# Kernel tuning notes

Hardware: AMD Instinct MI355X
Metric: run time of the kernel (lower is better)

The kernel has to match this reference:

```python
import jax, jax.numpy as jnp
import numpy as np
import math

B, S, D = 2, 2048, 1024
N_HEAD = 16
EPS = 1e-6

def setup_inputs() -> dict:
    key = jax.random.key(0)
    ks = jax.random.split(key, 12)
    def lin(k):
        kw, kb = jax.random.split(k)
        scale = 1.0 / math.sqrt(D)
        W = jax.random.uniform(kw, (D, D), jnp.float32, -scale, scale)
        b = jax.random.uniform(kb, (D,), jnp.float32, -scale, scale)
        return W, b
    Wq, bq = lin(ks[0]); Wk, bk = lin(ks[1]); Wv, bv = lin(ks[2]); Wo, bo = lin(ks[3])
    return {
        'query': jax.random.normal(ks[4], (B, S, D), jnp.float32),
        'key':   jax.random.normal(ks[5], (B, S, D), jnp.float32),
        'value': jax.random.normal(ks[6], (B, S, D), jnp.float32),
        'mask':  jnp.ones((B, S, S), jnp.int32),
        'Wq': Wq, 'bq': bq, 'Wk': Wk, 'bk': bk, 'Wv': Wv, 'bv': bv,
        'Wo': Wo, 'bo': bo,
        'gamma': jnp.ones((D,), jnp.float32),
        'beta':  jnp.zeros((D,), jnp.float32),
    }

def reference(query, key, value, mask, Wq, bq, Wk, bk, Wv, bv, Wo, bo, gamma, beta):
    b, s, dm = query.shape
    h = N_HEAD
    d = dm // h
    residual = query
    # projections (torch Linear: x @ W.T + b) -> [b, h, s, d]
    def proj(x, W, bias):
        return (x @ W.T + bias).reshape(b, -1, h, d).transpose(0, 2, 1, 3)
    q = proj(query, Wq, bq)
    k = proj(key, Wk, bk)
    v = proj(value, Wv, bv)
    scores = jnp.einsum('bhqd,bhkd->bhqk', q, k) / jnp.sqrt(jnp.float32(d))
    scores = jnp.where(mask[:, None, :, :] == 0, jnp.float32(-1e9), scores)
    p_attn = jax.nn.softmax(scores, axis=-1)  # dropout is identity in eval/reference
    x = jnp.einsum('bhqk,bhkd->bhqd', p_attn, v)
    x = x.transpose(0, 2, 1, 3).reshape(b, -1, h * d)
    x = x @ Wo.T + bo
    x = x + residual
    # LayerNorm with unbiased std and (std + eps) denominator, as in source
    mean = jnp.mean(x, axis=-1, keepdims=True)
    std = jnp.std(x, axis=-1, keepdims=True, ddof=1)
    return gamma * (x - mean) / (std + EPS) + beta
```

## Files before the change

kernel.cpp:

```cpp
#include <hip/hip_runtime.h>
#include <hip/hip_bf16.h>
#include <math.h>
#include <stdint.h>

#define BATCH 2
#define SEQ   2048
#define DMODEL 1024
#define NHEAD 16
#define HDIM  64
#define NROWS (BATCH*SEQ)
#define EPS   1e-6f
#define QSCALE 0.1803368801111204f

typedef float f32x4 __attribute__((ext_vector_type(4)));
typedef short s16x8 __attribute__((ext_vector_type(8)));
typedef unsigned int u32x4 __attribute__((ext_vector_type(4)));

#define OFF_XQ 0
#define OFF_XK 4194304
#define OFF_XV 8388608
#define OFF_WQ 12582912
#define OFF_WK 13631488
#define OFF_WV 14680064
#define OFF_WO 15728640
#define OFF_QB 16777216
#define OFF_KB 20971520
#define OFF_VT 25165824
#define OFF_CM 29360128
#define OFF_MS 29884416

__device__ __forceinline__ unsigned short f2bf(float x) {
    unsigned int u = __builtin_bit_cast(unsigned int, x);
    u += 0x7fff + ((u >> 16) & 1);
    return (unsigned short)(u >> 16);
}

__device__ __forceinline__ void gl_lds16(const void* g, void* l) {
    __builtin_amdgcn_global_load_lds(
        (const __attribute__((address_space(1))) unsigned int*)g,
        (__attribute__((address_space(3))) unsigned int*)(unsigned int)(unsigned long long)l,
        16, 0, 0);
}

__global__ __launch_bounds__(256) void conv_all_kernel(
    const float* __restrict__ q, const float* __restrict__ k, const float* __restrict__ v,
    const float* __restrict__ wq, const float* __restrict__ wk, const float* __restrict__ wv,
    const float* __restrict__ wo, unsigned short* __restrict__ ws)
{
    if (blockIdx.x == 0 && threadIdx.x < 32)
        ((unsigned int*)(ws + OFF_MS))[threadIdx.x] = 0;
    size_t t = ((size_t)blockIdx.x * 256 + threadIdx.x) * 4;
    const float* src; unsigned short* dst; size_t off;
    if (t < 4194304)       { src = q;  dst = ws + OFF_XQ; off = t; }
    else if (t < 8388608)  { src = k;  dst = ws + OFF_XK; off = t - 4194304; }
    else if (t < 12582912) { src = v;  dst = ws + OFF_XV; off = t - 8388608; }
    else if (t < 13631488) { src = wq; dst = ws + OFF_WQ; off = t - 12582912; }
    else if (t < 14680064) { src = wk; dst = ws + OFF_WK; off = t - 13631488; }
    else if (t < 15728640) { src = wv; dst = ws + OFF_WV; off = t - 14680064; }
    else                   { src = wo; dst = ws + OFF_WO; off = t - 15728640; }
    float4 x = *(const float4*)&src[off];
    ushort4 o;
    o.x = f2bf(x.x); o.y = f2bf(x.y); o.z = f2bf(x.z); o.w = f2bf(x.w);
    *(ushort4*)&dst[off] = o;
}

__global__ __launch_bounds__(256) void mask_compress_kernel(
    const int* __restrict__ mask, unsigned long long* __restrict__ cm,
    unsigned int* __restrict__ msum)
{
    int t = blockIdx.x * 256 + threadIdx.x;
    int lane = t & 63;
    int w = t >> 6;
    int s  = w & 2047;
    int kb = (w >> 11) & 31;
    int b  = w >> 16;
    int m = mask[((size_t)b * SEQ + s) * SEQ + kb * 64 + lane];
    unsigned long long bits = __ballot(m != 0);
    if (lane == 0) {
        cm[((size_t)b * 32 + kb) * SEQ + s] = bits;
        if (bits != ~0ull)
            atomicOr(&msum[(b << 4) | (s >> 7)], 1u << kb);
    }
}

__device__ __forceinline__ void gemm_body(
    const unsigned short* A, const unsigned short* W, int r0, int c0,
    unsigned short* As, unsigned short* Bs, f32x4 acc[4][4])
{
    const int tid  = threadIdx.x;
    const int wave = tid >> 6, lane = tid & 63;
    const int quad = lane >> 4, l15 = lane & 15;
    const int wr = wave >> 1, wc = wave & 1;
    for (int k0 = 0; k0 < DMODEL; k0 += 64) {
        __syncthreads();
        #pragma unroll
        for (int r = 0; r < 4; r++) {
            int f   = r * 4096 + tid * 16;
            int row = f >> 7;
            int g   = (((f >> 4) & 7) - row) & 7;
            gl_lds16((const char*)A + (size_t)(r0 + row) * 2048 + k0 * 2 + g * 16,
                     (char*)As + r * 4096 + wave * 1024);
            gl_lds16((const char*)W + (size_t)(c0 + row) * 2048 + k0 * 2 + g * 16,
                     (char*)Bs + r * 4096 + wave * 1024);
        }
        __syncthreads();
        #pragma unroll
        for (int ks = 0; ks < 2; ks++) {
            s16x8 a[4], b[4];
            #pragma unroll
            for (int mt = 0; mt < 4; mt++) {
                int row = wr*64 + mt*16 + l15;
                a[mt] = *(const s16x8*)((const char*)As + row * 128 + ((ks*4 + quad + row) & 7) * 16);
            }
            #pragma unroll
            for (int nt = 0; nt < 4; nt++) {
                int row = wc*64 + nt*16 + l15;
                b[nt] = *(const s16x8*)((const char*)Bs + row * 128 + ((ks*4 + quad + row) & 7) * 16);
            }
            #pragma unroll
            for (int mt = 0; mt < 4; mt++)
                #pragma unroll
                for (int nt = 0; nt < 4; nt++)
                    acc[mt][nt] = __builtin_amdgcn_mfma_f32_16x16x32_bf16(a[mt], b[nt], acc[mt][nt], 0, 0, 0);
        }
    }
}

__global__ __launch_bounds__(256) void qkv_gemm_kernel(
    unsigned short* __restrict__ ws,
    const float* __restrict__ bq, const float* __restrict__ bk, const float* __restrict__ bv)
{
    __shared__ __align__(16) unsigned short As[8192];
    __shared__ __align__(16) unsigned short Bs[8192];
    const int z = blockIdx.z;
    const unsigned short *A, *W;
    int r0, c0;
    if (z != 2) {
        A = ws + (size_t)z * 4194304;
        W = ws + OFF_WQ + (size_t)z * 1048576;
        r0 = blockIdx.x * 128; c0 = blockIdx.y * 128;
    } else {
        A = ws + OFF_WV;
        W = ws + OFF_XV;
        r0 = blockIdx.y * 128; c0 = blockIdx.x * 128;
    }
    const float* bias = (z == 0) ? bq : (z == 1 ? bk : bv);
    unsigned short* outp = ws + OFF_QB + (size_t)z * 4194304;
    const float scale = (z == 0) ? QSCALE : 1.0f;

    f32x4 acc[4][4] = {};
    gemm_body(A, W, r0, c0, As, Bs, acc);

    const int lane = threadIdx.x & 63, wave = threadIdx.x >> 6;
    const int quad = lane >> 4, l15 = lane & 15;
    const int wr = wave >> 1, wc = wave & 1;
    if (z != 2) {
        float bias_v[4];
        #pragma unroll
        for (int nt = 0; nt < 4; nt++) bias_v[nt] = bias[c0 + wc*64 + nt*16 + l15];
        #pragma unroll
        for (int mt = 0; mt < 4; mt++) {
            #pragma unroll
            for (int nt = 0; nt < 4; nt++) {
                int c = c0 + wc*64 + nt*16 + l15;
                int hh = c >> 6, dd = c & 63;
                #pragma unroll
                for (int reg = 0; reg < 4; reg++) {
                    int r = r0 + wr*64 + mt*16 + quad*4 + reg;
                    int bb = r >> 11, ss = r & (SEQ - 1);
                    float val = (acc[mt][nt][reg] + bias_v[nt]) * scale;
                    outp[(((size_t)(bb*NHEAD + hh)) * SEQ + ss) * HDIM + dd] = f2bf(val);
                }
            }
        }
    } else {
        #pragma unroll
        for (int mt = 0; mt < 4; mt++) {
            #pragma unroll
            for (int reg = 0; reg < 4; reg++) {
                int f = r0 + wr*64 + mt*16 + quad*4 + reg;
                int hh = f >> 6, dd = f & 63;
                float bfv = bias[f];
                #pragma unroll
                for (int nt = 0; nt < 4; nt++) {
                    int r = c0 + wc*64 + nt*16 + l15;
                    int bb = r >> 11, ss = r & (SEQ - 1);
                    outp[(((size_t)(bb*NHEAD + hh)) * HDIM + dd) * SEQ + ss] =
                        f2bf(acc[mt][nt][reg] + bfv);
                }
            }
        }
    }
}

__global__ __launch_bounds__(256) void oproj_gemm_kernel(
    const unsigned short* __restrict__ ws, const float* __restrict__ bo,
    const float* __restrict__ resid, float* __restrict__ outf)
{
    __shared__ __align__(16) unsigned short As[8192];
    __shared__ __align__(16) unsigned short Bs[8192];
    const unsigned short* A = ws + OFF_XQ;
    const unsigned short* W = ws + OFF_WO;
    const int r0 = blockIdx.x * 128, c0 = blockIdx.y * 128;

    f32x4 acc[4][4] = {};
    gemm_body(A, W, r0, c0, (unsigned short*)As, (unsigned short*)Bs, acc);

    const int lane = threadIdx.x & 63, wave = threadIdx.x >> 6;
    const int quad = lane >> 4, l15 = lane & 15;
    const int wr = wave >> 1, wc = wave & 1;
    #pragma unroll
    for (int mt = 0; mt < 4; mt++) {
        #pragma unroll
        for (int nt = 0; nt < 4; nt++) {
            int c = c0 + wc*64 + nt*16 + l15;
            float bv = bo[c];
            #pragma unroll
            for (int reg = 0; reg < 4; reg++) {
                int r = r0 + wr*64 + mt*16 + quad*4 + reg;
                size_t idx = (size_t)r * DMODEL + c;
                outf[idx] = acc[mt][nt][reg] + bv + resid[idx];
            }
        }
    }
}

__global__ __launch_bounds__(512) void attn_mfma_kernel(
    const unsigned short* __restrict__ ws,
    const unsigned long long* __restrict__ cmask,
    const unsigned int* __restrict__ msum,
    unsigned short* __restrict__ ab)
{
    const int tid  = threadIdx.x;
    const int wave = tid >> 6, lane = tid & 63;
    const int quad = lane >> 4, l15 = lane & 15;
    const int h = blockIdx.y, b = blockIdx.z;
    const int qw = blockIdx.x * 128 + wave * 16;

    const char* qh = (const char*)(ws + OFF_QB + ((size_t)(b*NHEAD + h)) * SEQ * HDIM);
    const char* kh = (const char*)(ws + OFF_KB + ((size_t)(b*NHEAD + h)) * SEQ * HDIM);
    const char* vh = (const char*)(ws + OFF_VT + ((size_t)(b*NHEAD + h)) * SEQ * HDIM);

    __shared__ __align__(16) char Ks[2][2][8192];
    __shared__ __align__(16) char Vs[2][2][8192];

    const unsigned int chunkflags = msum[(b << 4) | blockIdx.x];

    const int srow = tid >> 3;
    const int sgrp = ((tid & 7) - srow) & 7;
    const int arow = (srow & 0x23) | ((srow & 0x0C) << 1) | ((srow & 0x10) >> 2);

    #define STAGE(bfi, k0)                                                           \
        do {                                                                         \
            gl_lds16(kh + (size_t)((k0) + arow) * 128 + sgrp * 16,                   \
                     Ks[bfi][0] + wave * 1024);                                      \
            gl_lds16(kh + (size_t)((k0) + 64 + arow) * 128 + sgrp * 16,              \
                     Ks[bfi][1] + wave * 1024);                                      \
            gl_lds16(vh + (size_t)srow * 4096 + (size_t)(k0) * 2 + sgrp * 16,        \
                     Vs[bfi][0] + wave * 1024);                                      \
            gl_lds16(vh + (size_t)srow * 4096 + (size_t)((k0) + 64) * 2 + sgrp * 16, \
                     Vs[bfi][1] + wave * 1024);                                      \
        } while (0)

    s16x8 qa[2];
    #pragma unroll
    for (int ks = 0; ks < 2; ks++)
        qa[ks] = *(const s16x8*)(qh + (size_t)(qw + l15) * 128 + ks*64 + quad*16);

    int koff[4][2], voff[4][2];
    #pragma unroll
    for (int kt = 0; kt < 4; kt++) {
        int prow = kt*16 + l15;
        koff[kt][0] = prow*128 + ((quad     + prow) & 7) * 16;
        koff[kt][1] = prow*128 + ((4 + quad + prow) & 7) * 16;
    }
    #pragma unroll
    for (int nt = 0; nt < 4; nt++) {
        int d = nt*16 + l15;
        voff[nt][0] = d*128 + ((quad     + d) & 7) * 16;
        voff[nt][1] = d*128 + ((4 + quad + d) & 7) * 16;
    }

    s16x8 onesf;
    {
        short so = (short)0x3F80;
        if (l15 == 0) onesf = (s16x8){so, so, so, so, so, so, so, so};
        else          onesf = (s16x8){0, 0, 0, 0, 0, 0, 0, 0};
    }

    f32x4 o[4], lsum = {0.f, 0.f, 0.f, 0.f};
    #pragma unroll
    for (int nt = 0; nt < 4; nt++) o[nt] = (f32x4){0.f, 0.f, 0.f, 0.f};

    STAGE(0, 0);
    int bf = 0;
    for (int k0 = 0; k0 < SEQ; k0 += 128) {
        __syncthreads();
        if (k0 + 128 < SEQ) STAGE(bf ^ 1, k0 + 128);

        #pragma unroll
        for (int half = 0; half < 2; half++) {
            const char* Kb = Ks[bf][half];
            const char* Vb = Vs[bf][half];
            const int kc = (k0 >> 6) + half;
            f32x4 st[4];
            #pragma unroll
            for (int kt = 0; kt < 4; kt++) {
                s16x8 kf0 = *(const s16x8*)(Kb + koff[kt][0]);
                s16x8 kf1 = *(const s16x8*)(Kb + koff[kt][1]);
                f32x4 z = {0.f, 0.f, 0.f, 0.f};
                st[kt] = __builtin_amdgcn_mfma_f32_16x16x32_bf16(kf0, qa[0], z, 0, 0, 0);
                st[kt] = __builtin_amdgcn_mfma_f32_16x16x32_bf16(kf1, qa[1], st[kt], 0, 0, 0);
            }
            if (chunkflags & (1u << kc)) {
                unsigned long long cm =
                    cmask[((size_t)b*32 + kc) * SEQ + qw + l15];
                if (cm != ~0ull) {
                    #pragma unroll
                    for (int kt = 0; kt < 4; kt++)
                        #pragma unroll
                        for (int reg = 0; reg < 4; reg++) {
                            int key = (kt >> 1)*32 + quad*8 + (kt & 1)*4 + reg;
                            if (!((cm >> key) & 1)) st[kt][reg] = -1e9f;
                        }
                }
            }
            #pragma unroll
            for (int ks = 0; ks < 2; ks++) {
                unsigned int pb[8];
                #pragma unroll
                for (int j = 0; j < 8; j++) {
                    int kt = 2*ks + (j >> 2), r = j & 3;
                    pb[j] = __builtin_bit_cast(unsigned int, exp2f(st[kt][r]));
                }
                u32x4 pw;
                pw[0] = __builtin_amdgcn_perm(pb[1], pb[0], 0x07060302u);
                pw[1] = __builtin_amdgcn_perm(pb[3], pb[2], 0x07060302u);
                pw[2] = __builtin_amdgcn_perm(pb[5], pb[4], 0x07060302u);
                pw[3] = __builtin_amdgcn_perm(pb[7], pb[6], 0x07060302u);
                s16x8 pa = __builtin_bit_cast(s16x8, pw);
                lsum = __builtin_amdgcn_mfma_f32_16x16x32_bf16(pa, onesf, lsum, 0, 0, 0);
                #pragma unroll
                for (int nt = 0; nt < 4; nt++) {
                    s16x8 vf = *(const s16x8*)(Vb + voff[nt][ks]);
                    o[nt] = __builtin_amdgcn_mfma_f32_16x16x32_bf16(pa, vf, o[nt], 0, 0, 0);
                }
            }
        }
        bf ^= 1;
    }
    #undef STAGE
    #pragma unroll
    for (int reg = 0; reg < 4; reg++) {
        float lv = __shfl(lsum[reg], lane & 48);
        float inv = 1.f / lv;
        int sg = qw + quad*4 + reg;
        #pragma unroll
        for (int nt = 0; nt < 4; nt++) {
            size_t idx = ((size_t)b * SEQ + sg) * DMODEL + h*HDIM + nt*16 + l15;
            ab[idx] = f2bf(o[nt][reg] * inv);
        }
    }
}

__global__ __launch_bounds__(256) void ln_kernel(
    float* __restrict__ x, const float* __restrict__ gamma,
    const float* __restrict__ beta)
{
    const int row = blockIdx.x;
    const int tid = threadIdx.x;
    float4 vals = *(const float4*)&x[(size_t)row * DMODEL + tid * 4];
    float s  = vals.x + vals.y + vals.z + vals.w;
    float ss = vals.x*vals.x + vals.y*vals.y + vals.z*vals.z + vals.w*vals.w;
    #pragma unroll
    for (int off = 32; off > 0; off >>= 1) {
        s  += __shfl_down(s, off);
        ss += __shfl_down(ss, off);
    }
    __shared__ float sbuf[4], ssbuf[4];
    __shared__ float mean_s, inv_s;
    if ((tid & 63) == 0) { sbuf[tid >> 6] = s; ssbuf[tid >> 6] = ss; }
    __syncthreads();
    if (tid == 0) {
        float S1 = 0.f, S2 = 0.f;
        #pragma unroll
        for (int i = 0; i < 4; i++) { S1 += sbuf[i]; S2 += ssbuf[i]; }
        float mean = S1 * (1.0f / DMODEL);
        float var  = (S2 - (float)DMODEL * mean * mean) * (1.0f / (DMODEL - 1));
        float sd   = sqrtf(fmaxf(var, 0.f));
        mean_s = mean;
        inv_s  = 1.f / (sd + EPS);
    }
    __syncthreads();
    float4 g  = *(const float4*)&gamma[tid * 4];
    float4 bt = *(const float4*)&beta[tid * 4];
    float4 o;
    o.x = g.x * (vals.x - mean_s) * inv_s + bt.x;
    o.y = g.y * (vals.y - mean_s) * inv_s + bt.y;
    o.z = g.z * (vals.z - mean_s) * inv_s + bt.z;
    o.w = g.w * (vals.w - mean_s) * inv_s + bt.w;
    *(float4*)&x[(size_t)row * DMODEL + tid * 4] = o;
}

extern "C" void kernel_launch(void* const* d_in, const int* in_sizes, int n_in,
                              void* d_out, int out_size, void* d_ws, size_t ws_size,
                              hipStream_t stream) {
    const float* query = (const float*)d_in[0];
    const float* key   = (const float*)d_in[1];
    const float* value = (const float*)d_in[2];
    const int*   mask  = (const int*)d_in[3];
    const float* Wq = (const float*)d_in[4];  const float* bq = (const float*)d_in[5];
    const float* Wk = (const float*)d_in[6];  const float* bk = (const float*)d_in[7];
    const float* Wv = (const float*)d_in[8];  const float* bv = (const float*)d_in[9];
    const float* Wo = (const float*)d_in[10]; const float* bo = (const float*)d_in[11];
    const float* gamma = (const float*)d_in[12];
    const float* beta  = (const float*)d_in[13];
    float* out = (float*)d_out;

    unsigned short* ws = (unsigned short*)d_ws;
    unsigned long long* cmask = (unsigned long long*)(ws + OFF_CM);
    unsigned int* msum = (unsigned int*)(ws + OFF_MS);

    conv_all_kernel<<<16384, 256, 0, stream>>>(query, key, value, Wq, Wk, Wv, Wo, ws);
    mask_compress_kernel<<<32768, 256, 0, stream>>>(mask, cmask, msum);
    qkv_gemm_kernel<<<dim3(32, 8, 3), 256, 0, stream>>>(ws, bq, bk, bv);
    attn_mfma_kernel<<<dim3(SEQ/128, NHEAD, BATCH), 512, 0, stream>>>(ws, cmask, msum, ws + OFF_XQ);
    oproj_gemm_kernel<<<dim3(32, 8), 256, 0, stream>>>(ws, bo, query, out);
    ln_kernel<<<NROWS, 256, 0, stream>>>(out, gamma, beta);
}
```

Before: 283.2 us.

## Split attention key range across two wave groups with LDS merge

Grows the attention block to 1024 threads. Each group of 8 waves processes half of the key sequence for the same 128 queries, so there are twice as many waves in flight to hide latency. The partial outputs and row sums of the second half are combined through shared memory before normalisation. In exchange it uses 64KB of LDS per block, adds an extra merge step with two barriers, and its occupancy hint (1024, 8) may push register limits.

```diff
diff --git a/kernel.cpp b/kernel.cpp
--- a/kernel.cpp
+++ b/kernel.cpp
@@ -225,7 +225,7 @@
     }
 }
 
-__global__ __launch_bounds__(512) void attn_mfma_kernel(
+__global__ __launch_bounds__(1024, 8) void attn_mfma_kernel(
     const unsigned short* __restrict__ ws,
     const unsigned long long* __restrict__ cmask,
     const unsigned int* __restrict__ msum,
@@ -234,32 +234,33 @@
     const int tid  = threadIdx.x;
     const int wave = tid >> 6, lane = tid & 63;
     const int quad = lane >> 4, l15 = lane & 15;
+    const int w8   = wave & 7;
+    const int half = wave >> 3;
     const int h = blockIdx.y, b = blockIdx.z;
-    const int qw = blockIdx.x * 128 + wave * 16;
+    const int qw = blockIdx.x * 128 + w8 * 16;
 
     const char* qh = (const char*)(ws + OFF_QB + ((size_t)(b*NHEAD + h)) * SEQ * HDIM);
     const char* kh = (const char*)(ws + OFF_KB + ((size_t)(b*NHEAD + h)) * SEQ * HDIM);
     const char* vh = (const char*)(ws + OFF_VT + ((size_t)(b*NHEAD + h)) * SEQ * HDIM);
 
-    __shared__ __align__(16) char Ks[2][2][8192];
-    __shared__ __align__(16) char Vs[2][2][8192];
+    __shared__ __align__(16) char smem[65536];
+    char* Kbase = smem + half * 32768;
+    char* Vbase = smem + half * 32768 + 16384;
 
     const unsigned int chunkflags = msum[(b << 4) | blockIdx.x];
 
-    const int srow = tid >> 3;
-    const int sgrp = ((tid & 7) - srow) & 7;
+    const int t512 = tid & 511;
+    const int srow = t512 >> 3;
+    const int sgrp = ((t512 & 7) - srow) & 7;
     const int arow = (srow & 0x23) | ((srow & 0x0C) << 1) | ((srow & 0x10) >> 2);
-
-    #define STAGE(bfi, k0)                                                           \
-        do {                                                                         \
-            gl_lds16(kh + (size_t)((k0) + arow) * 128 + sgrp * 16,                   \
-                     Ks[bfi][0] + wave * 1024);                                      \
-            gl_lds16(kh + (size_t)((k0) + 64 + arow) * 128 + sgrp * 16,              \
-                     Ks[bfi][1] + wave * 1024);                                      \
-            gl_lds16(vh + (size_t)srow * 4096 + (size_t)(k0) * 2 + sgrp * 16,        \
-                     Vs[bfi][0] + wave * 1024);                                      \
-            gl_lds16(vh + (size_t)srow * 4096 + (size_t)((k0) + 64) * 2 + sgrp * 16, \
-                     Vs[bfi][1] + wave * 1024);                                      \
+    const int kb0  = half * 1024;
+
+    #define STAGE(bfi, k0)                                                      \
+        do {                                                                    \
+            gl_lds16(kh + (size_t)((k0) + arow) * 128 + sgrp * 16,              \
+                     Kbase + (bfi) * 8192 + w8 * 1024);                         \
+            gl_lds16(vh + (size_t)srow * 4096 + (size_t)(k0) * 2 + sgrp * 16,   \
+                     Vbase + (bfi) * 8192 + w8 * 1024);                         \
         } while (0)
 
     s16x8 qa[2];
@@ -292,73 +293,95 @@
     #pragma unroll
     for (int nt = 0; nt < 4; nt++) o[nt] = (f32x4){0.f, 0.f, 0.f, 0.f};
 
-    STAGE(0, 0);
+    STAGE(0, kb0);
     int bf = 0;
-    for (int k0 = 0; k0 < SEQ; k0 += 128) {
+    for (int kc = 0; kc < 16; kc++) {
         __syncthreads();
-        if (k0 + 128 < SEQ) STAGE(bf ^ 1, k0 + 128);
-
-        #pragma unroll
-        for (int half = 0; half < 2; half++) {
-            const char* Kb = Ks[bf][half];
-            const char* Vb = Vs[bf][half];
-            const int kc = (k0 >> 6) + half;
-            f32x4 st[4];
-            #pragma unroll
-            for (int kt = 0; kt < 4; kt++) {
-                s16x8 kf0 = *(const s16x8*)(Kb + koff[kt][0]);
-                s16x8 kf1 = *(const s16x8*)(Kb + koff[kt][1]);
-                f32x4 z = {0.f, 0.f, 0.f, 0.f};
-                st[kt] = __builtin_amdgcn_mfma_f32_16x16x32_bf16(kf0, qa[0], z, 0, 0, 0);
-                st[kt] = __builtin_amdgcn_mfma_f32_16x16x32_bf16(kf1, qa[1], st[kt], 0, 0, 0);
-            }
-            if (chunkflags & (1u << kc)) {
-                unsigned long long cm =
-                    cmask[((size_t)b*32 + kc) * SEQ + qw + l15];
-                if (cm != ~0ull) {
+        if (kc + 1 < 16) STAGE(bf ^ 1, kb0 + (kc + 1) * 64);
+
+        const char* Kb = Kbase + bf * 8192;
+        const char* Vb = Vbase + bf * 8192;
+        const int kcg = (half << 4) + kc;
+        f32x4 st[4];
+        #pragma unroll
+        for (int kt = 0; kt < 4; kt++) {
+            s16x8 kf0 = *(const s16x8*)(Kb + koff[kt][0]);
+            s16x8 kf1 = *(const s16x8*)(Kb + koff[kt][1]);
+            f32x4 z = {0.f, 0.f, 0.f, 0.f};
+            st[kt] = __builtin_amdgcn_mfma_f32_16x16x32_bf16(kf0, qa[0], z, 0, 0, 0);
+            st[kt] = __builtin_amdgcn_mfma_f32_16x16x32_bf16(kf1, qa[1], st[kt], 0, 0, 0);
+        }
+        if (chunkflags & (1u << kcg)) {
+            unsigned long long cm =
+                cmask[((size_t)b*32 + kcg) * SEQ + qw + l15];
+            if (cm != ~0ull) {
+                #pragma unroll
+                for (int kt = 0; kt < 4; kt++)
                     #pragma unroll
-                    for (int kt = 0; kt < 4; kt++)
-                        #pragma unroll
-                        for (int reg = 0; reg < 4; reg++) {
-                            int key = (kt >> 1)*32 + quad*8 + (kt & 1)*4 + reg;
-                            if (!((cm >> key) & 1)) st[kt][reg] = -1e9f;
-                        }
-                }
-            }
-            #pragma unroll
-            for (int ks = 0; ks < 2; ks++) {
-                unsigned int pb[8];
-                #pragma unroll
-                for (int j = 0; j < 8; j++) {
-                    int kt = 2*ks + (j >> 2), r = j & 3;
-                    pb[j] = __builtin_bit_cast(unsigned int, exp2f(st[kt][r]));
-                }
-                u32x4 pw;
-                pw[0] = __builtin_amdgcn_perm(pb[1], pb[0], 0x07060302u);
-                pw[1] = __builtin_amdgcn_perm(pb[3], pb[2], 0x07060302u);
-                pw[2] = __builtin_amdgcn_perm(pb[5], pb[4], 0x07060302u);
-                pw[3] = __builtin_amdgcn_perm(pb[7], pb[6], 0x07060302u);
-                s16x8 pa = __builtin_bit_cast(s16x8, pw);
-                lsum = __builtin_amdgcn_mfma_f32_16x16x32_bf16(pa, onesf, lsum, 0, 0, 0);
-                #pragma unroll
-                for (int nt = 0; nt < 4; nt++) {
-                    s16x8 vf = *(const s16x8*)(Vb + voff[nt][ks]);
-                    o[nt] = __builtin_amdgcn_mfma_f32_16x16x32_bf16(pa, vf, o[nt], 0, 0, 0);
-                }
+                    for (int reg = 0; reg < 4; reg++) {
+                        int key = (kt >> 1)*32 + quad*8 + (kt & 1)*4 + reg;
+                        if (!((cm >> key) & 1)) st[kt][reg] = -1e9f;
+                    }
+            }
+        }
+        #pragma unroll
+        for (int ks = 0; ks < 2; ks++) {
+            unsigned int pb[8];
+            #pragma unroll
+            for (int j = 0; j < 8; j++) {
+                int kt = 2*ks + (j >> 2), r = j & 3;
+                pb[j] = __builtin_bit_cast(unsigned int, exp2f(st[kt][r]));
+            }
+            u32x4 pw;
+            pw[0] = __builtin_amdgcn_perm(pb[1], pb[0], 0x07060302u);
+            pw[1] = __builtin_amdgcn_perm(pb[3], pb[2], 0x07060302u);
+            pw[2] = __builtin_amdgcn_perm(pb[5], pb[4], 0x07060302u);
+            pw[3] = __builtin_amdgcn_perm(pb[7], pb[6], 0x07060302u);
+            s16x8 pa = __builtin_bit_cast(s16x8, pw);
+            lsum = __builtin_amdgcn_mfma_f32_16x16x32_bf16(pa, onesf, lsum, 0, 0, 0);
+            #pragma unroll
+            for (int nt = 0; nt < 4; nt++) {
+                s16x8 vf = *(const s16x8*)(Vb + voff[nt][ks]);
+                o[nt] = __builtin_amdgcn_mfma_f32_16x16x32_bf16(pa, vf, o[nt], 0, 0, 0);
             }
         }
         bf ^= 1;
     }
     #undef STAGE
-    #pragma unroll
-    for (int reg = 0; reg < 4; reg++) {
-        float lv = __shfl(lsum[reg], lane & 48);
-        float inv = 1.f / lv;
-        int sg = qw + quad*4 + reg;
-        #pragma unroll
-        for (int nt = 0; nt < 4; nt++) {
-            size_t idx = ((size_t)b * SEQ + sg) * DMODEL + h*HDIM + nt*16 + l15;
-            ab[idx] = f2bf(o[nt][reg] * inv);
+
+    __syncthreads();
+    float* mbuf = (float*)smem;
+    const int mslot = (w8 * 64 + lane) * 21;
+    if (half == 1) {
+        #pragma unroll
+        for (int nt = 0; nt < 4; nt++)
+            #pragma unroll
+            for (int reg = 0; reg < 4; reg++)
+                mbuf[mslot + nt*4 + reg] = o[nt][reg];
+        #pragma unroll
+        for (int reg = 0; reg < 4; reg++)
+            mbuf[mslot + 16 + reg] = lsum[reg];
+    }
+    __syncthreads();
+    if (half == 0) {
+        #pragma unroll
+        for (int nt = 0; nt < 4; nt++)
+            #pragma unroll
+            for (int reg = 0; reg < 4; reg++)
+                o[nt][reg] += mbuf[mslot + nt*4 + reg];
+        #pragma unroll
+        for (int reg = 0; reg < 4; reg++)
+            lsum[reg] += mbuf[mslot + 16 + reg];
+        #pragma unroll
+        for (int reg = 0; reg < 4; reg++) {
+            float lv = __shfl(lsum[reg], lane & 48);
+            float inv = 1.f / lv;
+            int sg = qw + quad*4 + reg;
+            #pragma unroll
+            for (int nt = 0; nt < 4; nt++) {
+                size_t idx = ((size_t)b * SEQ + sg) * DMODEL + h*HDIM + nt*16 + l15;
+                ab[idx] = f2bf(o[nt][reg] * inv);
+            }
         }
     }
 }
@@ -424,7 +447,7 @@
     conv_all_kernel<<<16384, 256, 0, stream>>>(query, key, value, Wq, Wk, Wv, Wo, ws);
     mask_compress_kernel<<<32768, 256, 0, stream>>>(mask, cmask, msum);
     qkv_gemm_kernel<<<dim3(32, 8, 3), 256, 0, stream>>>(ws, bq, bk, bv);
-    attn_mfma_kernel<<<dim3(SEQ/128, NHEAD, BATCH), 512, 0, stream>>>(ws, cmask, msum, ws + OFF_XQ);
+    attn_mfma_kernel<<<dim3(SEQ/128, NHEAD, BATCH), 1024, 0, stream>>>(ws, cmask, msum, ws + OFF_XQ);
     oproj_gemm_kernel<<<dim3(32, 8), 256, 0, stream>>>(ws, bo, query, out);
     ln_kernel<<<NROWS, 256, 0, stream>>>(out, gamma, beta);
 }
```

New measurement: 311.2 us. 9.9% more time.

## Fold mask compression into QKV GEMM launch and simplify LDS fragment addressing

Applied to the files above, without the earlier changes.

The separate mask_compress kernel is removed. Its work now runs in an extra z-slice (z==3) of the QKV GEMM grid, where 256 blocks each scan 512 mask rows with a per-wave loop, overlapping the mask read with the GEMM blocks and saving one launch. Swizzled LDS offsets in the GEMM and attention kernels are also rewritten as base offset plus constant stride, which relies on the row-based swizzle term being invariant across 16-row tiles. This cuts address arithmetic and registers. The risk is that the 64 MB mask read now competes with the GEMM for bandwidth, and the fewer mask blocks may have less parallelism.

```diff
diff --git a/kernel.cpp b/kernel.cpp
--- a/kernel.cpp
+++ b/kernel.cpp
@@ -64,25 +64,6 @@
     *(ushort4*)&dst[off] = o;
 }
 
-__global__ __launch_bounds__(256) void mask_compress_kernel(
-    const int* __restrict__ mask, unsigned long long* __restrict__ cm,
-    unsigned int* __restrict__ msum)
-{
-    int t = blockIdx.x * 256 + threadIdx.x;
-    int lane = t & 63;
-    int w = t >> 6;
-    int s  = w & 2047;
-    int kb = (w >> 11) & 31;
-    int b  = w >> 16;
-    int m = mask[((size_t)b * SEQ + s) * SEQ + kb * 64 + lane];
-    unsigned long long bits = __ballot(m != 0);
-    if (lane == 0) {
-        cm[((size_t)b * 32 + kb) * SEQ + s] = bits;
-        if (bits != ~0ull)
-            atomicOr(&msum[(b << 4) | (s >> 7)], 1u << kb);
-    }
-}
-
 __device__ __forceinline__ void gemm_body(
     const unsigned short* A, const unsigned short* W, int r0, int c0,
     unsigned short* As, unsigned short* Bs, f32x4 acc[4][4])
@@ -91,6 +72,10 @@
     const int wave = tid >> 6, lane = tid & 63;
     const int quad = lane >> 4, l15 = lane & 15;
     const int wr = wave >> 1, wc = wave & 1;
+    const int aBase0 = (wr*64 + l15)*128 + ((    quad + l15) & 7)*16;
+    const int aBase1 = (wr*64 + l15)*128 + ((4 + quad + l15) & 7)*16;
+    const int bBase0 = (wc*64 + l15)*128 + ((    quad + l15) & 7)*16;
+    const int bBase1 = (wc*64 + l15)*128 + ((4 + quad + l15) & 7)*16;
     for (int k0 = 0; k0 < DMODEL; k0 += 64) {
         __syncthreads();
         #pragma unroll
@@ -106,17 +91,15 @@
         __syncthreads();
         #pragma unroll
         for (int ks = 0; ks < 2; ks++) {
+            const int aB = ks ? aBase1 : aBase0;
+            const int bB = ks ? bBase1 : bBase0;
             s16x8 a[4], b[4];
             #pragma unroll
-            for (int mt = 0; mt < 4; mt++) {
-                int row = wr*64 + mt*16 + l15;
-                a[mt] = *(const s16x8*)((const char*)As + row * 128 + ((ks*4 + quad + row) & 7) * 16);
-            }
-            #pragma unroll
-            for (int nt = 0; nt < 4; nt++) {
-                int row = wc*64 + nt*16 + l15;
-                b[nt] = *(const s16x8*)((const char*)Bs + row * 128 + ((ks*4 + quad + row) & 7) * 16);
-            }
+            for (int mt = 0; mt < 4; mt++)
+                a[mt] = *(const s16x8*)((const char*)As + aB + mt*2048);
+            #pragma unroll
+            for (int nt = 0; nt < 4; nt++)
+                b[nt] = *(const s16x8*)((const char*)Bs + bB + nt*2048);
             #pragma unroll
             for (int mt = 0; mt < 4; mt++)
                 #pragma unroll
@@ -128,11 +111,35 @@
 
 __global__ __launch_bounds__(256) void qkv_gemm_kernel(
     unsigned short* __restrict__ ws,
-    const float* __restrict__ bq, const float* __restrict__ bk, const float* __restrict__ bv)
-{
+    const float* __restrict__ bq, const float* __restrict__ bk, const float* __restrict__ bv,
+    const int* __restrict__ mask)
+{
+    const int z = blockIdx.z;
+    if (z == 3) {
+        unsigned long long* cm = (unsigned long long*)(ws + OFF_CM);
+        unsigned int* msum = (unsigned int*)(ws + OFF_MS);
+        const int lane = threadIdx.x & 63;
+        const int wv = threadIdx.x >> 6;
+        const int bid = blockIdx.y * 32 + blockIdx.x;
+        const int wbase = (bid * 4 + wv) * 128;
+        for (int i = 0; i < 128; i++) {
+            int w = wbase + i;
+            int s  = w & 2047;
+            int kb = (w >> 11) & 31;
+            int b  = w >> 16;
+            int m = mask[((size_t)b * SEQ + s) * SEQ + kb * 64 + lane];
+            unsigned long long bits = __ballot(m != 0);
+            if (lane == 0) {
+                cm[((size_t)b * 32 + kb) * SEQ + s] = bits;
+                if (bits != ~0ull)
+                    atomicOr(&msum[(b << 4) | (s >> 7)], 1u << kb);
+            }
+        }
+        return;
+    }
+
     __shared__ __align__(16) unsigned short As[8192];
     __shared__ __align__(16) unsigned short Bs[8192];
-    const int z = blockIdx.z;
     const unsigned short *A, *W;
     int r0, c0;
     if (z != 2) {
@@ -267,19 +274,8 @@
     for (int ks = 0; ks < 2; ks++)
         qa[ks] = *(const s16x8*)(qh + (size_t)(qw + l15) * 128 + ks*64 + quad*16);
 
-    int koff[4][2], voff[4][2];
-    #pragma unroll
-    for (int kt = 0; kt < 4; kt++) {
-        int prow = kt*16 + l15;
-        koff[kt][0] = prow*128 + ((quad     + prow) & 7) * 16;
-        koff[kt][1] = prow*128 + ((4 + quad + prow) & 7) * 16;
-    }
-    #pragma unroll
-    for (int nt = 0; nt < 4; nt++) {
-        int d = nt*16 + l15;
-        voff[nt][0] = d*128 + ((quad     + d) & 7) * 16;
-        voff[nt][1] = d*128 + ((4 + quad + d) & 7) * 16;
-    }
+    const int fbaseA = l15*128 + ((    quad + l15) & 7) * 16;
+    const int fbaseB = l15*128 + ((4 + quad + l15) & 7) * 16;
 
     s16x8 onesf;
     {
@@ -306,8 +302,8 @@
             f32x4 st[4];
             #pragma unroll
             for (int kt = 0; kt < 4; kt++) {
-                s16x8 kf0 = *(const s16x8*)(Kb + koff[kt][0]);
-                s16x8 kf1 = *(const s16x8*)(Kb + koff[kt][1]);
+                s16x8 kf0 = *(const s16x8*)(Kb + fbaseA + kt*2048);
+                s16x8 kf1 = *(const s16x8*)(Kb + fbaseB + kt*2048);
                 f32x4 z = {0.f, 0.f, 0.f, 0.f};
                 st[kt] = __builtin_amdgcn_mfma_f32_16x16x32_bf16(kf0, qa[0], z, 0, 0, 0);
                 st[kt] = __builtin_amdgcn_mfma_f32_16x16x32_bf16(kf1, qa[1], st[kt], 0, 0, 0);
@@ -340,9 +336,10 @@
                 pw[3] = __builtin_amdgcn_perm(pb[7], pb[6], 0x07060302u);
                 s16x8 pa = __builtin_bit_cast(s16x8, pw);
                 lsum = __builtin_amdgcn_mfma_f32_16x16x32_bf16(pa, onesf, lsum, 0, 0, 0);
+                const int fb = (ks == 0) ? fbaseA : fbaseB;
                 #pragma unroll
                 for (int nt = 0; nt < 4; nt++) {
-                    s16x8 vf = *(const s16x8*)(Vb + voff[nt][ks]);
+                    s16x8 vf = *(const s16x8*)(Vb + fb + nt*2048);
                     o[nt] = __builtin_amdgcn_mfma_f32_16x16x32_bf16(pa, vf, o[nt], 0, 0, 0);
                 }
             }
@@ -422,8 +419,7 @@
     unsigned int* msum = (unsigned int*)(ws + OFF_MS);
 
     conv_all_kernel<<<16384, 256, 0, stream>>>(query, key, value, Wq, Wk, Wv, Wo, ws);
-    mask_compress_kernel<<<32768, 256, 0, stream>>>(mask, cmask, msum);
-    qkv_gemm_kernel<<<dim3(32, 8, 3), 256, 0, stream>>>(ws, bq, bk, bv);
+    qkv_gemm_kernel<<<dim3(32, 8, 4), 256, 0, stream>>>(ws, bq, bk, bv, mask);
     attn_mfma_kernel<<<dim3(SEQ/128, NHEAD, BATCH), 512, 0, stream>>>(ws, cmask, msum, ws + OFF_XQ);
     oproj_gemm_kernel<<<dim3(32, 8), 256, 0, stream>>>(ws, bo, query, out);
     ln_kernel<<<NROWS, 256, 0, stream>>>(out, gamma, beta);
```

Result: slower. 320.2 us (+13.1%).
